# Kernel tuning notes

Hardware: AMD Instinct MI355X
Metric: run time of the kernel (lower is better)

Reference implementation:

```python
import jax, jax.numpy as jnp
import numpy as np

G = 1024   # number of glimpses
P = 1024   # points per glimpse
N = G * P  # total points


def _pool(pos, batch, start, size):
    """voxel_mean_pool index computation: unique (batch, voxel) cells."""
    vox = np.floor((pos - start) / size).astype(np.int64)
    vox -= vox.min(axis=0)
    dims = vox.max(axis=0) + 1
    key = ((batch * dims[0] + vox[:, 0]) * dims[1] + vox[:, 1]) * dims[2] + vox[:, 2]
    uniq, first, inv = np.unique(key, return_index=True, return_inverse=True)
    return inv.astype(np.int64), batch[first].astype(np.int64), int(uniq.shape[0])


def setup_inputs() -> dict:
    rng = np.random.default_rng(0)
    pos = rng.uniform(-1.0, 1.0, (N, 3)).astype(np.float32)
    rgb = rng.random((N, 1)).astype(np.float32)
    batch = np.repeat(np.arange(G, dtype=np.int64), P)
    # min_pos gets a random negative offset (noise) in the torch code
    min_pos = pos.min(axis=0) - rng.random(3).astype(np.float32)
    # level-1 voxel pooling (size 0.25)
    cluster1, batch1, M1 = _pool(pos, batch, min_pos, 0.25)
    cnt1 = np.bincount(cluster1, minlength=M1).astype(np.float32)[:, None]
    ps1 = np.zeros((M1, 3), np.float32)
    np.add.at(ps1, cluster1, pos)
    ps1 /= cnt1
    # level-2 voxel pooling (size 0.5) on voxel centers
    cluster2, batch2, M2 = _pool(ps1, batch1, min_pos, 0.5)

    def lin(fi, fo):
        return (rng.standard_normal((fi, fo)).astype(np.float32) / np.sqrt(fi))

    d = dict(
        rgb=jnp.asarray(rgb), pos=jnp.asarray(pos),
        glimpse_center=jnp.asarray(rng.standard_normal((G, 3)).astype(np.float32)),
        W1l=jnp.asarray(lin(1 + 3, 16)), b1l=jnp.zeros(16, jnp.float32),
        W1g=jnp.asarray(lin(16, 32)), b1g=jnp.zeros(32, jnp.float32),
        W2l=jnp.asarray(lin(32 + 3, 64)), b2l=jnp.zeros(64, jnp.float32),
        W2g=jnp.asarray(lin(64, 128)), b2g=jnp.zeros(128, jnp.float32),
        W3l=jnp.asarray(lin(128 + 3, 128)), b3l=jnp.zeros(128, jnp.float32),
        W3g=jnp.asarray(lin(128, 256)), b3g=jnp.zeros(256, jnp.float32),
        Wlin=jnp.asarray(lin(256, 256)), blin=jnp.zeros(256, jnp.float32),
        eps=jnp.asarray(rng.standard_normal((G, 128)).astype(np.float32)),
        glimpse_index=jnp.asarray(batch),
        cluster1=jnp.asarray(cluster1), cluster2=jnp.asarray(cluster2),
        batch2=jnp.asarray(batch2),
        num_voxels1=M1, num_voxels2=M2,
    )
    return d


def _seg_mean(x, seg, m):
    s = jax.ops.segment_sum(x, seg, num_segments=m)
    c = jax.ops.segment_sum(jnp.ones((x.shape[0], 1), x.dtype), seg, num_segments=m)
    return s / jnp.maximum(c, 1.0)


def _point_conv(x_in, pos_in, pos_out, out_index, Wl, bl, Wg, bg, m_out):
    # gather: relative position of each input point to its output (voxel) center
    rel = pos_in - pos_out[out_index]                      # [E,3]
    msg = jax.nn.relu(jnp.concatenate([x_in, rel], 1) @ Wl + bl)  # [E,c_mid]
    agg = jax.ops.segment_max(msg, out_index, num_segments=m_out)  # [M,c_mid]
    return agg @ Wg + bg


def reference(rgb, pos, glimpse_center, W1l, b1l, W1g, b1g, W2l, b2l, W2g, b2g,
              W3l, b3l, W3g, b3g, Wlin, blin, eps, glimpse_index,
              cluster1, cluster2, batch2, num_voxels1, num_voxels2):
    M1, M2 = num_voxels1, num_voxels2
    Gn = glimpse_center.shape[0]
    # stage 1: voxel mean pool (0.25) + PointConv 1->16->32
    ps1 = _seg_mean(pos, cluster1, M1)                     # [M1,3]
    f1 = jax.nn.celu(_point_conv(rgb, pos, ps1, cluster1, W1l, b1l, W1g, b1g, M1))
    # stage 2: voxel mean pool (0.5) + PointConv 32->64->128
    ps2 = _seg_mean(ps1, cluster2, M2)                     # [M2,3]
    f2 = jax.nn.celu(_point_conv(f1, ps1, ps2, cluster2, W2l, b2l, W2g, b2g, M2))
    # stage 3: pool everything to the glimpse center (pos_out = zeros)
    pos_out = jnp.zeros_like(glimpse_center)
    f3 = jax.nn.celu(_point_conv(f2, ps2, pos_out, batch2, W3l, b3l, W3g, b3g, Gn))
    # head: Linear(256,256), split into mu/sigma, reparameterized sample
    out = f3 @ Wlin + blin                                 # [G,256]
    mu, s = jnp.split(out, 2, axis=1)
    sigma = jax.nn.softplus(s)
    z = mu + sigma * eps                                   # [G,128]
    z_what, z_mask = jnp.split(z, 2, axis=1)
    return z_what, z_mask, mu, sigma, f3
```

## Files before the change

### kernel.cpp

```cpp
#include <hip/hip_runtime.h>
#include <math.h>

#define N1CAP 736
#define N2CAP 192
#define S3 132

__device__ __forceinline__ float celu1(float x){ return x > 0.f ? x : (__expf(x) - 1.f); }
__device__ __forceinline__ float softplus1(float x){ return fmaxf(x, 0.f) + log1pf(__expf(-fabsf(x))); }
__device__ __forceinline__ void atomicMaxNonneg(float* p, float v){
    atomicMax((int*)p, __float_as_int(v));
}

__global__ __launch_bounds__(256) void kA(const float* __restrict__ rgb,
                                          const float* __restrict__ pos,
                                          const int* __restrict__ cl1,
                                          const float* __restrict__ W1l,
                                          const float* __restrict__ b1l,
                                          float* __restrict__ ps1,
                                          float* __restrict__ agg1,
                                          float* __restrict__ cnt1,
                                          int* __restrict__ seg1, int P){
    __shared__ float sp[3*1024];
    __shared__ float srgb[1024];
    __shared__ int   ci[1024];
    __shared__ int   cnt[N1CAP];
    __shared__ int   start[N1CAP+1];
    __shared__ int   cur[N1CAP];
    __shared__ unsigned short pidx[1024];
    __shared__ float wsh[64], bsh[16];
    __shared__ int   red[2];
    __shared__ int   wsum[4];
    const int g = blockIdx.x, tid = threadIdx.x;
    const int base = g * P;
    const bool pfit = (P <= 1024);

    if (tid == 0){ red[0] = 0x7fffffff; red[1] = -1; }
    if (tid < 64) wsh[tid] = W1l[tid];
    if (tid < 16) bsh[tid] = b1l[tid];
    __syncthreads();
    int mn = 0x7fffffff, mx = -1;
    for (int i = tid; i < P; i += 256){
        int c = cl1[base+i];
        if (pfit) ci[i] = c;
        mn = min(mn,c); mx = max(mx,c);
    }
    atomicMin(&red[0], mn); atomicMax(&red[1], mx);
    __syncthreads();
    const int s1 = red[0];
    const int n1 = red[1] - red[0] + 1;
    const bool fast = pfit && (n1 <= N1CAP);

    if (fast){
        for (int t = tid; t < 3*P; t += 256) sp[t] = pos[(size_t)base*3 + t];
        for (int t = tid; t < P;   t += 256) srgb[t] = rgb[base + t];
        for (int l = tid; l < n1;  l += 256) cnt[l] = 0;
        __syncthreads();
        for (int i = tid; i < P; i += 256) atomicAdd(&cnt[ci[i] - s1], 1);
        __syncthreads();
        {
            int b3 = tid*3;
            int a0 = (b3   < n1) ? cnt[b3]   : 0;
            int a1 = (b3+1 < n1) ? cnt[b3+1] : 0;
            int a2 = (b3+2 < n1) ? cnt[b3+2] : 0;
            int s = a0+a1+a2;
            int lane = tid & 63, wv = tid >> 6;
            int ps = s;
            #pragma unroll
            for (int d = 1; d < 64; d <<= 1){
                int t2 = __shfl_up(ps, d, 64);
                if (lane >= d) ps += t2;
            }
            if (lane == 63) wsum[wv] = ps;
            __syncthreads();
            int woff = 0;
            #pragma unroll
            for (int w = 0; w < 4; ++w) woff += (w < wv) ? wsum[w] : 0;
            int excl = woff + ps - s;
            if (b3   < n1){ start[b3]   = excl;       cur[b3]   = excl; }
            if (b3+1 < n1){ start[b3+1] = excl+a0;    cur[b3+1] = excl+a0; }
            if (b3+2 < n1){ start[b3+2] = excl+a0+a1; cur[b3+2] = excl+a0+a1; }
            if (tid == 0) start[n1] = P;
        }
        __syncthreads();
        for (int i = tid; i < P; i += 256){
            int slot = atomicAdd(&cur[ci[i] - s1], 1);
            pidx[slot] = (unsigned short)i;
        }
        __syncthreads();
        for (int l = tid; l < n1; l += 256){
            int s0 = start[l], e0 = start[l+1];
            float sxv=0.f, syv=0.f, szv=0.f;
            for (int k = s0; k < e0; ++k){
                int i = pidx[k];
                sxv += sp[3*i+0]; syv += sp[3*i+1]; szv += sp[3*i+2];
            }
            float ic = 1.0f / (float)max(e0 - s0, 1);
            float mxp = sxv*ic, myp = syv*ic, mzp = szv*ic;
            ps1[(size_t)(s1+l)*3+0] = mxp;
            ps1[(size_t)(s1+l)*3+1] = myp;
            ps1[(size_t)(s1+l)*3+2] = mzp;
            float acc[16];
            #pragma unroll
            for (int j = 0; j < 16; ++j) acc[j] = 0.f;
            for (int k = s0; k < e0; ++k){
                int i = pidx[k];
                float in0 = srgb[i];
                float r0 = sp[3*i+0] - mxp;
                float r1 = sp[3*i+1] - myp;
                float r2 = sp[3*i+2] - mzp;
                #pragma unroll
                for (int j = 0; j < 16; ++j){
                    float v = bsh[j] + in0*wsh[j] + r0*wsh[16+j] + r1*wsh[32+j] + r2*wsh[48+j];
                    acc[j] = fmaxf(acc[j], fmaxf(v, 0.f));
                }
            }
            float4* dst = (float4*)&agg1[(size_t)(s1+l)*16];
            dst[0] = make_float4(acc[0], acc[1], acc[2], acc[3]);
            dst[1] = make_float4(acc[4], acc[5], acc[6], acc[7]);
            dst[2] = make_float4(acc[8], acc[9], acc[10], acc[11]);
            dst[3] = make_float4(acc[12], acc[13], acc[14], acc[15]);
        }
    } else {
        for (int t = tid; t < n1;    t += 256) cnt1[s1+t] = 0.f;
        for (int t = tid; t < n1*3;  t += 256) ps1[(size_t)s1*3+t] = 0.f;
        for (int t = tid; t < n1*16; t += 256) agg1[(size_t)s1*16+t] = 0.f;
        __syncthreads();
        for (int i = tid; i < P; i += 256){
            int idx = base + i; int c = cl1[idx];
            atomicAdd(&ps1[3*c+0], pos[3*idx+0]);
            atomicAdd(&ps1[3*c+1], pos[3*idx+1]);
            atomicAdd(&ps1[3*c+2], pos[3*idx+2]);
            atomicAdd(&cnt1[c], 1.0f);
        }
        __syncthreads();
        for (int l = tid; l < n1; l += 256){
            float ic = 1.0f / fmaxf(cnt1[s1+l], 1.0f);
            ps1[(size_t)(s1+l)*3+0] *= ic; ps1[(size_t)(s1+l)*3+1] *= ic; ps1[(size_t)(s1+l)*3+2] *= ic;
        }
        __syncthreads();
        for (int i = tid; i < P; i += 256){
            int idx = base + i; int c = cl1[idx];
            float in0 = rgb[idx];
            float r0 = pos[3*idx+0] - ps1[3*c+0];
            float r1 = pos[3*idx+1] - ps1[3*c+1];
            float r2 = pos[3*idx+2] - ps1[3*c+2];
            #pragma unroll
            for (int j = 0; j < 16; ++j){
                float v = b1l[j] + in0*W1l[j] + r0*W1l[16+j] + r1*W1l[32+j] + r2*W1l[48+j];
                atomicMaxNonneg(&agg1[(size_t)c*16+j], fmaxf(v, 0.0f));
            }
        }
    }
    if (tid == 0){ seg1[2*g] = s1; seg1[2*g+1] = n1; }
}

__global__ __launch_bounds__(256) void kB(const float* __restrict__ ps1,
                                          const float* __restrict__ agg1,
                                          const int* __restrict__ cl2,
                                          const float* __restrict__ W1g,
                                          const float* __restrict__ b1g,
                                          const float* __restrict__ W2l,
                                          const float* __restrict__ b2l,
                                          const int* __restrict__ seg1,
                                          float* __restrict__ ps2,
                                          float* __restrict__ agg2,
                                          float* __restrict__ cnt2,
                                          int* __restrict__ seg2){
    __shared__ float sx[N2CAP], sy[N2CAP], sz[N2CAP], sc[N2CAP];
    __shared__ float sagg[N2CAP*64];
    __shared__ int red[2];
    const int g = blockIdx.x, tid = threadIdx.x;
    const int s1 = seg1[2*g], n1 = seg1[2*g+1], e1 = s1 + n1;

    if (tid == 0){ red[0] = 0x7fffffff; red[1] = -1; }
    __syncthreads();
    int mn = 0x7fffffff, mx = -1;
    for (int m = s1 + tid; m < e1; m += 256){ int c = cl2[m]; mn = min(mn,c); mx = max(mx,c); }
    atomicMin(&red[0], mn); atomicMax(&red[1], mx);
    __syncthreads();
    const int s2 = red[0];
    const int n2 = red[1] - red[0] + 1;
    const bool fast = (n2 <= N2CAP);

    if (fast){
        for (int l = tid; l < n2; l += 256){ sx[l]=0.f; sy[l]=0.f; sz[l]=0.f; sc[l]=0.f; }
        for (int t = tid; t < n2*64; t += 256) sagg[t] = 0.f;
        __syncthreads();
        for (int m = s1 + tid; m < e1; m += 256){
            int c = cl2[m] - s2;
            atomicAdd(&sx[c], ps1[3*m+0]);
            atomicAdd(&sy[c], ps1[3*m+1]);
            atomicAdd(&sz[c], ps1[3*m+2]);
            atomicAdd(&sc[c], 1.0f);
        }
        __syncthreads();
        for (int l = tid; l < n2; l += 256){
            float ic = 1.0f / sc[l];
            sx[l] *= ic; sy[l] *= ic; sz[l] *= ic;
        }
        __syncthreads();
        for (int t = tid; t < n2*3; t += 256){
            int l = t/3, d = t - 3*l;
            ps2[(size_t)s2*3 + t] = (d==0) ? sx[l] : ((d==1) ? sy[l] : sz[l]);
        }
        for (int m = s1 + tid; m < e1; m += 256){
            float a[16];
            const float* ar = agg1 + (size_t)m*16;
            #pragma unroll
            for (int k = 0; k < 16; ++k) a[k] = ar[k];
            float in[35];
            for (int j = 0; j < 32; j += 4){
                float v0=b1g[j+0], v1=b1g[j+1], v2=b1g[j+2], v3=b1g[j+3];
                #pragma unroll
                for (int k = 0; k < 16; ++k){
                    float x = a[k];
                    const float* w = &W1g[k*32 + j];
                    v0 += x*w[0]; v1 += x*w[1]; v2 += x*w[2]; v3 += x*w[3];
                }
                in[j+0]=celu1(v0); in[j+1]=celu1(v1); in[j+2]=celu1(v2); in[j+3]=celu1(v3);
            }
            int c = cl2[m] - s2;
            in[32] = ps1[3*m+0] - sx[c];
            in[33] = ps1[3*m+1] - sy[c];
            in[34] = ps1[3*m+2] - sz[c];
            float* dst = &sagg[c*64];
            for (int j = 0; j < 64; j += 4){
                float v0=b2l[j+0], v1=b2l[j+1], v2=b2l[j+2], v3=b2l[j+3];
                #pragma unroll
                for (int k = 0; k < 35; ++k){
                    float x = in[k];
                    const float* w = &W2l[k*64 + j];
                    v0 += x*w[0]; v1 += x*w[1]; v2 += x*w[2]; v3 += x*w[3];
                }
                atomicMaxNonneg(&dst[(j+0 + c) & 63], fmaxf(v0, 0.0f));
                atomicMaxNonneg(&dst[(j+1 + c) & 63], fmaxf(v1, 0.0f));
                atomicMaxNonneg(&dst[(j+2 + c) & 63], fmaxf(v2, 0.0f));
                atomicMaxNonneg(&dst[(j+3 + c) & 63], fmaxf(v3, 0.0f));
            }
        }
        __syncthreads();
        for (int t = tid; t < n2*64; t += 256){
            int l = t >> 6, j = t & 63;
            agg2[(size_t)s2*64 + t] = sagg[l*64 + ((j + l) & 63)];
        }
    } else {
        for (int t = tid; t < n2;    t += 256) cnt2[s2+t] = 0.f;
        for (int t = tid; t < n2*3;  t += 256) ps2[(size_t)s2*3+t] = 0.f;
        for (int t = tid; t < n2*64; t += 256) agg2[(size_t)s2*64+t] = 0.f;
        __syncthreads();
        for (int m = s1 + tid; m < e1; m += 256){
            int c = cl2[m];
            atomicAdd(&ps2[3*c+0], ps1[3*m+0]);
            atomicAdd(&ps2[3*c+1], ps1[3*m+1]);
            atomicAdd(&ps2[3*c+2], ps1[3*m+2]);
            atomicAdd(&cnt2[c], 1.0f);
        }
        __syncthreads();
        for (int l = tid; l < n2; l += 256){
            float ic = 1.0f / fmaxf(cnt2[s2+l], 1.0f);
            ps2[(size_t)(s2+l)*3+0] *= ic; ps2[(size_t)(s2+l)*3+1] *= ic; ps2[(size_t)(s2+l)*3+2] *= ic;
        }
        __syncthreads();
        for (int m = s1 + tid; m < e1; m += 256){
            float a[16];
            const float* ar = agg1 + (size_t)m*16;
            #pragma unroll
            for (int k = 0; k < 16; ++k) a[k] = ar[k];
            float in[35];
            #pragma unroll 1
            for (int j = 0; j < 32; ++j){
                float v = b1g[j];
                #pragma unroll 4
                for (int k = 0; k < 16; ++k) v += a[k] * W1g[k*32+j];
                in[j] = celu1(v);
            }
            int c = cl2[m];
            in[32] = ps1[3*m+0] - ps2[3*c+0];
            in[33] = ps1[3*m+1] - ps2[3*c+1];
            in[34] = ps1[3*m+2] - ps2[3*c+2];
            #pragma unroll 1
            for (int j = 0; j < 64; ++j){
                float v = b2l[j];
                #pragma unroll 5
                for (int k = 0; k < 35; ++k) v += in[k] * W2l[k*64+j];
                atomicMaxNonneg(&agg2[(size_t)c*64+j], fmaxf(v, 0.0f));
            }
        }
    }
    if (tid == 0){ seg2[2*g] = s2; seg2[2*g+1] = n2; }
}

__global__ __launch_bounds__(256) void k_f2f(const float* __restrict__ agg2,
                                             const float* __restrict__ W2g,
                                             const float* __restrict__ b2g,
                                             float* __restrict__ f2, int M2){
    __shared__ float Ws[64*128];
    __shared__ float xt[32*S3];
    const int tid = threadIdx.x;
    const int m0 = blockIdx.x * 128;
    for (int t = tid; t < 64*128; t += 256) Ws[t] = W2g[t];
    const int tr = tid & 31, tc = tid >> 5;
    float acc[4][16];
    #pragma unroll
    for (int c = 0; c < 16; ++c){
        float b = b2g[tc*16 + c];
        #pragma unroll
        for (int r = 0; r < 4; ++r) acc[r][c] = b;
    }
    for (int c0 = 0; c0 < 64; c0 += 32){
        __syncthreads();
        for (int t = tid; t < 128*8; t += 256){
            int row = t >> 3, kq = t & 7;
            int m = m0 + row;
            float4 v = (m < M2) ? *(const float4*)&agg2[(size_t)m*64 + c0 + kq*4]
                                : make_float4(0.f,0.f,0.f,0.f);
            xt[(kq*4+0)*S3 + row] = v.x;
            xt[(kq*4+1)*S3 + row] = v.y;
            xt[(kq*4+2)*S3 + row] = v.z;
            xt[(kq*4+3)*S3 + row] = v.w;
        }
        __syncthreads();
        #pragma unroll 4
        for (int kk = 0; kk < 32; ++kk){
            int k = c0 + kk;
            float4 xr = *(const float4*)&xt[kk*S3 + tr*4];
            float xv[4] = {xr.x, xr.y, xr.z, xr.w};
            float wv[16];
            #pragma unroll
            for (int q = 0; q < 4; ++q){
                float4 w = *(const float4*)&Ws[k*128 + tc*16 + q*4];
                wv[q*4+0]=w.x; wv[q*4+1]=w.y; wv[q*4+2]=w.z; wv[q*4+3]=w.w;
            }
            #pragma unroll
            for (int r = 0; r < 4; ++r)
                #pragma unroll
                for (int c = 0; c < 16; ++c) acc[r][c] += xv[r]*wv[c];
        }
    }
    #pragma unroll
    for (int r = 0; r < 4; ++r){
        int m = m0 + tr*4 + r;
        if (m < M2){
            #pragma unroll
            for (int q = 0; q < 4; ++q){
                float4 o;
                o.x = celu1(acc[r][q*4+0]); o.y = celu1(acc[r][q*4+1]);
                o.z = celu1(acc[r][q*4+2]); o.w = celu1(acc[r][q*4+3]);
                *(float4*)&f2[(size_t)m*128 + tc*16 + q*4] = o;
            }
        }
    }
}

__global__ __launch_bounds__(256) void k_msg3g(const float* __restrict__ f2,
                                               const float* __restrict__ ps2,
                                               const int* __restrict__ seg2,
                                               const float* __restrict__ W3l,
                                               const float* __restrict__ b3l,
                                               float* __restrict__ agg3, int G){
    __shared__ float Wh[131*64];
    __shared__ float xt[32*S3];
    __shared__ float shAgg[256];
    const int tid = threadIdx.x;
    const int cb = blockIdx.y * 64;
    const int g0 = blockIdx.x * 4;
    const int S  = seg2[2*g0];
    int n0 = seg2[2*g0+1];
    int nA = (g0+1 < G) ? seg2[2*(g0+1)+1] : 0;
    int nB = (g0+2 < G) ? seg2[2*(g0+2)+1] : 0;
    int nC = (g0+3 < G) ? seg2[2*(g0+3)+1] : 0;
    const int B1 = n0, B2 = B1 + nA, B3 = B2 + nB, T = B3 + nC;
    for (int t = tid; t < 131*64; t += 256){
        int k = t >> 6, c = t & 63;
        Wh[t] = W3l[k*128 + cb + c];
    }
    shAgg[tid] = 0.f;
    const int tr = tid & 31, tc = tid >> 5;
    float bias[8];
    #pragma unroll
    for (int c = 0; c < 8; ++c) bias[c] = b3l[cb + tc*8 + c];

    for (int w0 = 0; w0 < T; w0 += 128){
        float acc[4][8];
        #pragma unroll
        for (int r = 0; r < 4; ++r)
            #pragma unroll
            for (int c = 0; c < 8; ++c) acc[r][c] = bias[c];
        for (int c0 = 0; c0 < 128; c0 += 32){
            __syncthreads();
            for (int t = tid; t < 128*8; t += 256){
                int row = t >> 3, kq = t & 7;
                int ridx = w0 + row;
                float4 v = (ridx < T) ? *(const float4*)&f2[(size_t)(S+ridx)*128 + c0 + kq*4]
                                      : make_float4(0.f,0.f,0.f,0.f);
                xt[(kq*4+0)*S3 + row] = v.x;
                xt[(kq*4+1)*S3 + row] = v.y;
                xt[(kq*4+2)*S3 + row] = v.z;
                xt[(kq*4+3)*S3 + row] = v.w;
            }
            __syncthreads();
            #pragma unroll 8
            for (int kk = 0; kk < 32; ++kk){
                int k = c0 + kk;
                float4 xr = *(const float4*)&xt[kk*S3 + tr*4];
                float xv[4] = {xr.x, xr.y, xr.z, xr.w};
                float4 wa = *(const float4*)&Wh[k*64 + tc*8];
                float4 wb = *(const float4*)&Wh[k*64 + tc*8 + 4];
                float wv[8] = {wa.x,wa.y,wa.z,wa.w, wb.x,wb.y,wb.z,wb.w};
                #pragma unroll
                for (int r = 0; r < 4; ++r)
                    #pragma unroll
                    for (int c = 0; c < 8; ++c) acc[r][c] += xv[r]*wv[c];
            }
        }
        #pragma unroll
        for (int kk = 0; kk < 3; ++kk){
            const float* w = &Wh[(128+kk)*64 + tc*8];
            float wv[8];
            #pragma unroll
            for (int c = 0; c < 8; ++c) wv[c] = w[c];
            #pragma unroll
            for (int r = 0; r < 4; ++r){
                int ridx = w0 + tr*4 + r;
                float x = (ridx < T) ? ps2[(size_t)(S+ridx)*3 + kk] : 0.f;
                #pragma unroll
                for (int c = 0; c < 8; ++c) acc[r][c] += x*wv[c];
            }
        }
        float mx[8];
        int cur = -1;
        #pragma unroll
        for (int r = 0; r < 4; ++r){
            int ridx = w0 + tr*4 + r;
            if (ridx < T){
                int loc = (ridx >= B1) + (ridx >= B2) + (ridx >= B3);
                if (loc != cur){
                    if (cur >= 0){
                        #pragma unroll
                        for (int c = 0; c < 8; ++c)
                            atomicMaxNonneg(&shAgg[cur*64 + tc*8 + c], mx[c]);
                    }
                    cur = loc;
                    #pragma unroll
                    for (int c = 0; c < 8; ++c) mx[c] = fmaxf(acc[r][c], 0.f);
                } else {
                    #pragma unroll
                    for (int c = 0; c < 8; ++c) mx[c] = fmaxf(mx[c], fmaxf(acc[r][c], 0.f));
                }
            }
        }
        if (cur >= 0){
            #pragma unroll
            for (int c = 0; c < 8; ++c)
                atomicMaxNonneg(&shAgg[cur*64 + tc*8 + c], mx[c]);
        }
    }
    __syncthreads();
    {
        int loc = tid >> 6, c = tid & 63;
        int g = g0 + loc;
        if (g < G)
            agg3[(size_t)g*128 + cb + c] = shAgg[loc*64 + c];
    }
}

__global__ __launch_bounds__(256) void k_head(const float* __restrict__ agg3,
                                              const float* __restrict__ W3g,
                                              const float* __restrict__ b3g,
                                              const float* __restrict__ Wlin,
                                              const float* __restrict__ blin,
                                              const float* __restrict__ eps,
                                              float* __restrict__ out, int G){
    __shared__ float a3[128];
    __shared__ float f3s[256];
    __shared__ float hs[256];
    int g = blockIdx.x;
    int j = threadIdx.x;
    if (j < 128) a3[j] = agg3[(size_t)g*128 + j];
    __syncthreads();

    float v = b3g[j];
    for (int k = 0; k < 128; ++k) v += a3[k] * W3g[k*256 + j];
    v = celu1(v);
    f3s[j] = v;
    const size_t o_zm = (size_t)64*G, o_mu = (size_t)128*G, o_sg = (size_t)256*G, o_f3 = (size_t)384*G;
    out[o_f3 + (size_t)g*256 + j] = v;
    __syncthreads();

    float h = blin[j];
    for (int k = 0; k < 256; ++k) h += f3s[k] * Wlin[k*256 + j];
    hs[j] = h;
    __syncthreads();

    if (j < 128){
        float mu = hs[j];
        float sg = softplus1(hs[128 + j]);
        float z = mu + sg * eps[(size_t)g*128 + j];
        out[o_mu + (size_t)g*128 + j] = mu;
        out[o_sg + (size_t)g*128 + j] = sg;
        if (j < 64) out[(size_t)g*64 + j] = z;
        else        out[o_zm + (size_t)g*64 + (j - 64)] = z;
    }
}

extern "C" void kernel_launch(void* const* d_in, const int* in_sizes, int n_in,
                              void* d_out, int out_size, void* d_ws, size_t ws_size,
                              hipStream_t stream) {
    const float* rgb  = (const float*)d_in[0];
    const float* pos  = (const float*)d_in[1];
    const float* W1l  = (const float*)d_in[3];
    const float* b1l  = (const float*)d_in[4];
    const float* W1g  = (const float*)d_in[5];
    const float* b1g  = (const float*)d_in[6];
    const float* W2l  = (const float*)d_in[7];
    const float* b2l  = (const float*)d_in[8];
    const float* W2g  = (const float*)d_in[9];
    const float* b2g  = (const float*)d_in[10];
    const float* W3l  = (const float*)d_in[11];
    const float* b3l  = (const float*)d_in[12];
    const float* W3g  = (const float*)d_in[13];
    const float* b3g  = (const float*)d_in[14];
    const float* Wlin = (const float*)d_in[15];
    const float* blin = (const float*)d_in[16];
    const float* eps  = (const float*)d_in[17];
    const int* cl1 = (const int*)d_in[19];
    const int* cl2 = (const int*)d_in[20];

    const int N  = in_sizes[19];
    const int G  = in_sizes[17] / 128;
    const int M1 = in_sizes[20];
    const int M2 = in_sizes[21];
    const int P  = N / G;

    char* ws = (char*)d_ws;
    auto al = [](size_t x){ return (x + 255) & ~(size_t)255; };
    size_t off = 0;
    float* ps1  = (float*)(ws + off); off = al(off + 12ull*M1);
    size_t uni  = ((size_t)64*M1 > (size_t)512*M2) ? (size_t)64*M1 : (size_t)512*M2;
    float* agg1 = (float*)(ws + off);
    float* f2   = (float*)(ws + off);
    off = al(off + uni);
    float* cnt1 = (float*)(ws + off); off = al(off + 4ull*M1);
    float* ps2  = (float*)(ws + off); off = al(off + 12ull*M2);
    float* agg2 = (float*)(ws + off); off = al(off + 256ull*M2);
    float* cnt2 = (float*)(ws + off); off = al(off + 4ull*M2);
    float* agg3 = (float*)(ws + off); off = al(off + 512ull*G);
    int*   seg1 = (int*)  (ws + off); off = al(off + 8ull*G);
    int*   seg2 = (int*)  (ws + off); off = al(off + 8ull*G);
    if (off > ws_size) return;

    kA<<<G, 256, 0, stream>>>(rgb, pos, cl1, W1l, b1l, ps1, agg1, cnt1, seg1, P);
    kB<<<G, 256, 0, stream>>>(ps1, agg1, cl2, W1g, b1g, W2l, b2l, seg1, ps2, agg2, cnt2, seg2);
    int gx = (M2 + 127) / 128;
    k_f2f  <<<gx, 256, 0, stream>>>(agg2, W2g, b2g, f2, M2);
    dim3 g3((G + 3) / 4, 2);
    k_msg3g<<<g3, 256, 0, stream>>>(f2, ps2, seg2, W3l, b3l, agg3, G);
    k_head <<<G, 256, 0, stream>>>(agg3, W3g, b3g, Wlin, blin, eps, (float*)d_out, G);
}
```

Baseline: 387.8 us.

## Split stage-2 pooling into own kernel and halve per-block work in kB and msg3

Moves the level-2 voxel mean pooling and segment bookkeeping out of kB into a new kernel kM, so kB reads ps2 and seg2 from global memory. kB now runs on a 2D grid, with each block computing 32 of the 64 output channels, which halves its shared-memory aggregation buffer and doubles the number of blocks. k_msg3g handles 2 glimpses per block instead of 4, again doubling the grid. The aim is more parallelism and occupancy. The cost is an extra launch, and each of the two kB halves recomputes the 16->32 layer for every point.

Result: slower. 463.9 us (+19.6%).

```diff
diff --git a/kernel.cpp b/kernel.cpp
--- a/kernel.cpp
+++ b/kernel.cpp
@@ -154,6 +154,63 @@
     if (tid == 0){ seg1[2*g] = s1; seg1[2*g+1] = n1; }
 }
 
+__global__ __launch_bounds__(256) void kM(const float* __restrict__ ps1,
+                                          const int* __restrict__ cl2,
+                                          const int* __restrict__ seg1,
+                                          float* __restrict__ ps2,
+                                          float* __restrict__ cnt2,
+                                          int* __restrict__ seg2){
+    __shared__ float sx[N2CAP], sy[N2CAP], sz[N2CAP], sc[N2CAP];
+    __shared__ int red[2];
+    const int g = blockIdx.x, tid = threadIdx.x;
+    const int s1 = seg1[2*g], n1 = seg1[2*g+1], e1 = s1 + n1;
+    if (tid == 0){ red[0] = 0x7fffffff; red[1] = -1; }
+    __syncthreads();
+    int mn = 0x7fffffff, mx = -1;
+    for (int m = s1 + tid; m < e1; m += 256){ int c = cl2[m]; mn = min(mn,c); mx = max(mx,c); }
+    atomicMin(&red[0], mn); atomicMax(&red[1], mx);
+    __syncthreads();
+    const int s2 = red[0], n2 = red[1] - red[0] + 1;
+    if (n2 <= N2CAP){
+        for (int l = tid; l < n2; l += 256){ sx[l]=0.f; sy[l]=0.f; sz[l]=0.f; sc[l]=0.f; }
+        __syncthreads();
+        for (int m = s1 + tid; m < e1; m += 256){
+            int c = cl2[m] - s2;
+            atomicAdd(&sx[c], ps1[3*m+0]);
+            atomicAdd(&sy[c], ps1[3*m+1]);
+            atomicAdd(&sz[c], ps1[3*m+2]);
+            atomicAdd(&sc[c], 1.0f);
+        }
+        __syncthreads();
+        for (int l = tid; l < n2; l += 256){
+            float ic = 1.0f / sc[l];
+            sx[l] *= ic; sy[l] *= ic; sz[l] *= ic;
+        }
+        __syncthreads();
+        for (int t = tid; t < n2*3; t += 256){
+            int l = t/3, d = t - 3*l;
+            ps2[(size_t)s2*3 + t] = (d==0) ? sx[l] : ((d==1) ? sy[l] : sz[l]);
+        }
+    } else {
+        for (int t = tid; t < n2;   t += 256) cnt2[s2+t] = 0.f;
+        for (int t = tid; t < n2*3; t += 256) ps2[(size_t)s2*3+t] = 0.f;
+        __syncthreads();
+        for (int m = s1 + tid; m < e1; m += 256){
+            int c = cl2[m];
+            atomicAdd(&ps2[3*c+0], ps1[3*m+0]);
+            atomicAdd(&ps2[3*c+1], ps1[3*m+1]);
+            atomicAdd(&ps2[3*c+2], ps1[3*m+2]);
+            atomicAdd(&cnt2[c], 1.0f);
+        }
+        __syncthreads();
+        for (int l = tid; l < n2; l += 256){
+            float ic = 1.0f / fmaxf(cnt2[s2+l], 1.0f);
+            ps2[(size_t)(s2+l)*3+0] *= ic; ps2[(size_t)(s2+l)*3+1] *= ic; ps2[(size_t)(s2+l)*3+2] *= ic;
+        }
+    }
+    if (tid == 0){ seg2[2*g] = s2; seg2[2*g+1] = n2; }
+}
+
 __global__ __launch_bounds__(256) void kB(const float* __restrict__ ps1,
                                           const float* __restrict__ agg1,
                                           const int* __restrict__ cl2,
@@ -162,47 +219,18 @@
                                           const float* __restrict__ W2l,
                                           const float* __restrict__ b2l,
                                           const int* __restrict__ seg1,
-                                          float* __restrict__ ps2,
-                                          float* __restrict__ agg2,
-                                          float* __restrict__ cnt2,
-                                          int* __restrict__ seg2){
-    __shared__ float sx[N2CAP], sy[N2CAP], sz[N2CAP], sc[N2CAP];
-    __shared__ float sagg[N2CAP*64];
-    __shared__ int red[2];
-    const int g = blockIdx.x, tid = threadIdx.x;
+                                          const int* __restrict__ seg2,
+                                          const float* __restrict__ ps2,
+                                          float* __restrict__ agg2){
+    __shared__ float sagg[N2CAP*32];
+    const int g = blockIdx.x, h = blockIdx.y, tid = threadIdx.x;
+    const int cbase = h * 32;
     const int s1 = seg1[2*g], n1 = seg1[2*g+1], e1 = s1 + n1;
-
-    if (tid == 0){ red[0] = 0x7fffffff; red[1] = -1; }
-    __syncthreads();
-    int mn = 0x7fffffff, mx = -1;
-    for (int m = s1 + tid; m < e1; m += 256){ int c = cl2[m]; mn = min(mn,c); mx = max(mx,c); }
-    atomicMin(&red[0], mn); atomicMax(&red[1], mx);
-    __syncthreads();
-    const int s2 = red[0];
-    const int n2 = red[1] - red[0] + 1;
-    const bool fast = (n2 <= N2CAP);
-
-    if (fast){
-        for (int l = tid; l < n2; l += 256){ sx[l]=0.f; sy[l]=0.f; sz[l]=0.f; sc[l]=0.f; }
-        for (int t = tid; t < n2*64; t += 256) sagg[t] = 0.f;
-        __syncthreads();
-        for (int m = s1 + tid; m < e1; m += 256){
-            int c = cl2[m] - s2;
-            atomicAdd(&sx[c], ps1[3*m+0]);
-            atomicAdd(&sy[c], ps1[3*m+1]);
-            atomicAdd(&sz[c], ps1[3*m+2]);
-            atomicAdd(&sc[c], 1.0f);
-        }
-        __syncthreads();
-        for (int l = tid; l < n2; l += 256){
-            float ic = 1.0f / sc[l];
-            sx[l] *= ic; sy[l] *= ic; sz[l] *= ic;
-        }
-        __syncthreads();
-        for (int t = tid; t < n2*3; t += 256){
-            int l = t/3, d = t - 3*l;
-            ps2[(size_t)s2*3 + t] = (d==0) ? sx[l] : ((d==1) ? sy[l] : sz[l]);
-        }
+    const int s2 = seg2[2*g], n2 = seg2[2*g+1];
+
+    if (n2 <= N2CAP){
+        for (int t = tid; t < n2*32; t += 256) sagg[t] = 0.f;
+        __syncthreads();
         for (int m = s1 + tid; m < e1; m += 256){
             float a[16];
             const float* ar = agg1 + (size_t)m*16;
@@ -219,47 +247,34 @@
                 }
                 in[j+0]=celu1(v0); in[j+1]=celu1(v1); in[j+2]=celu1(v2); in[j+3]=celu1(v3);
             }
-            int c = cl2[m] - s2;
-            in[32] = ps1[3*m+0] - sx[c];
-            in[33] = ps1[3*m+1] - sy[c];
-            in[34] = ps1[3*m+2] - sz[c];
-            float* dst = &sagg[c*64];
-            for (int j = 0; j < 64; j += 4){
-                float v0=b2l[j+0], v1=b2l[j+1], v2=b2l[j+2], v3=b2l[j+3];
+            int cg = cl2[m];
+            int c = cg - s2;
+            in[32] = ps1[3*m+0] - ps2[3*cg+0];
+            in[33] = ps1[3*m+1] - ps2[3*cg+1];
+            in[34] = ps1[3*m+2] - ps2[3*cg+2];
+            float* dst = &sagg[c*32];
+            for (int j = 0; j < 32; j += 4){
+                float v0=b2l[cbase+j+0], v1=b2l[cbase+j+1], v2=b2l[cbase+j+2], v3=b2l[cbase+j+3];
                 #pragma unroll
                 for (int k = 0; k < 35; ++k){
                     float x = in[k];
-                    const float* w = &W2l[k*64 + j];
+                    const float* w = &W2l[k*64 + cbase + j];
                     v0 += x*w[0]; v1 += x*w[1]; v2 += x*w[2]; v3 += x*w[3];
                 }
-                atomicMaxNonneg(&dst[(j+0 + c) & 63], fmaxf(v0, 0.0f));
-                atomicMaxNonneg(&dst[(j+1 + c) & 63], fmaxf(v1, 0.0f));
-                atomicMaxNonneg(&dst[(j+2 + c) & 63], fmaxf(v2, 0.0f));
-                atomicMaxNonneg(&dst[(j+3 + c) & 63], fmaxf(v3, 0.0f));
-            }
-        }
-        __syncthreads();
-        for (int t = tid; t < n2*64; t += 256){
-            int l = t >> 6, j = t & 63;
-            agg2[(size_t)s2*64 + t] = sagg[l*64 + ((j + l) & 63)];
+                atomicMaxNonneg(&dst[(j+0 + c) & 31], fmaxf(v0, 0.0f));
+                atomicMaxNonneg(&dst[(j+1 + c) & 31], fmaxf(v1, 0.0f));
+                atomicMaxNonneg(&dst[(j+2 + c) & 31], fmaxf(v2, 0.0f));
+                atomicMaxNonneg(&dst[(j+3 + c) & 31], fmaxf(v3, 0.0f));
+            }
+        }
+        __syncthreads();
+        for (int t = tid; t < n2*32; t += 256){
+            int l = t >> 5, j = t & 31;
+            agg2[(size_t)(s2+l)*64 + cbase + j] = sagg[l*32 + ((j + l) & 31)];
         }
     } else {
-        for (int t = tid; t < n2;    t += 256) cnt2[s2+t] = 0.f;
-        for (int t = tid; t < n2*3;  t += 256) ps2[(size_t)s2*3+t] = 0.f;
+        if (h == 1) return;
         for (int t = tid; t < n2*64; t += 256) agg2[(size_t)s2*64+t] = 0.f;
-        __syncthreads();
-        for (int m = s1 + tid; m < e1; m += 256){
-            int c = cl2[m];
-            atomicAdd(&ps2[3*c+0], ps1[3*m+0]);
-            atomicAdd(&ps2[3*c+1], ps1[3*m+1]);
-            atomicAdd(&ps2[3*c+2], ps1[3*m+2]);
-            atomicAdd(&cnt2[c], 1.0f);
-        }
-        __syncthreads();
-        for (int l = tid; l < n2; l += 256){
-            float ic = 1.0f / fmaxf(cnt2[s2+l], 1.0f);
-            ps2[(size_t)(s2+l)*3+0] *= ic; ps2[(size_t)(s2+l)*3+1] *= ic; ps2[(size_t)(s2+l)*3+2] *= ic;
-        }
         __syncthreads();
         for (int m = s1 + tid; m < e1; m += 256){
             float a[16];
@@ -287,7 +302,6 @@
             }
         }
     }
-    if (tid == 0){ seg2[2*g] = s2; seg2[2*g+1] = n2; }
 }
 
 __global__ __launch_bounds__(256) void k_f2f(const float* __restrict__ agg2,
@@ -360,21 +374,19 @@
                                                float* __restrict__ agg3, int G){
     __shared__ float Wh[131*64];
     __shared__ float xt[32*S3];
-    __shared__ float shAgg[256];
+    __shared__ float shAgg[128];
     const int tid = threadIdx.x;
     const int cb = blockIdx.y * 64;
-    const int g0 = blockIdx.x * 4;
+    const int g0 = blockIdx.x * 2;
     const int S  = seg2[2*g0];
     int n0 = seg2[2*g0+1];
     int nA = (g0+1 < G) ? seg2[2*(g0+1)+1] : 0;
-    int nB = (g0+2 < G) ? seg2[2*(g0+2)+1] : 0;
-    int nC = (g0+3 < G) ? seg2[2*(g0+3)+1] : 0;
-    const int B1 = n0, B2 = B1 + nA, B3 = B2 + nB, T = B3 + nC;
+    const int B1 = n0, T = B1 + nA;
     for (int t = tid; t < 131*64; t += 256){
         int k = t >> 6, c = t & 63;
         Wh[t] = W3l[k*128 + cb + c];
     }
-    shAgg[tid] = 0.f;
+    if (tid < 128) shAgg[tid] = 0.f;
     const int tr = tid & 31, tc = tid >> 5;
     float bias[8];
     #pragma unroll
@@ -433,7 +445,7 @@
         for (int r = 0; r < 4; ++r){
             int ridx = w0 + tr*4 + r;
             if (ridx < T){
-                int loc = (ridx >= B1) + (ridx >= B2) + (ridx >= B3);
+                int loc = (ridx >= B1) ? 1 : 0;
                 if (loc != cur){
                     if (cur >= 0){
                         #pragma unroll
@@ -456,7 +468,7 @@
         }
     }
     __syncthreads();
-    {
+    if (tid < 128){
         int loc = tid >> 6, c = tid & 63;
         int g = g0 + loc;
         if (g < G)
@@ -550,10 +562,12 @@
     if (off > ws_size) return;
 
     kA<<<G, 256, 0, stream>>>(rgb, pos, cl1, W1l, b1l, ps1, agg1, cnt1, seg1, P);
-    kB<<<G, 256, 0, stream>>>(ps1, agg1, cl2, W1g, b1g, W2l, b2l, seg1, ps2, agg2, cnt2, seg2);
+    kM<<<G, 256, 0, stream>>>(ps1, cl2, seg1, ps2, cnt2, seg2);
+    dim3 gB(G, 2);
+    kB<<<gB, 256, 0, stream>>>(ps1, agg1, cl2, W1g, b1g, W2l, b2l, seg1, seg2, ps2, agg2);
     int gx = (M2 + 127) / 128;
     k_f2f  <<<gx, 256, 0, stream>>>(agg2, W2g, b2g, f2, M2);
-    dim3 g3((G + 3) / 4, 2);
+    dim3 g3((G + 1) / 2, 2);
     k_msg3g<<<g3, 256, 0, stream>>>(f2, ps2, seg2, W3l, b3l, agg3, G);
     k_head <<<G, 256, 0, stream>>>(agg3, W3g, b3g, Wlin, blin, eps, (float*)d_out, G);
 }
```
